# Performance work log

Measured on AMD Instinct MI355X. Metric: run time of the kernel, lower is better.

The kernel has to match this reference:

```python
import jax, jax.numpy as jnp
import numpy as np

B, T, E, D, H = 32, 2048, 512, 1024, 128

def setup_inputs() -> dict:
    key = jax.random.key(0)
    ks = jax.random.split(key, 8)
    encoder_outs = jax.random.normal(ks[0], (B, T, E), dtype=jnp.float32)
    decoder_state = jax.random.normal(ks[1], (B, D), dtype=jnp.float32)
    # valid lengths in [T//2, T]; mask=True on padded positions
    src_lens = jnp.clip(jax.random.randint(ks[2], (B,), 0, T), T // 2, T).astype(jnp.int32)
    mask = jnp.arange(T)[None, :] >= src_lens[:, None]  # [B,T] bool
    # parameters (nn.Linear style: y = x @ W^T + b; here stored pre-transposed)
    W_enc = jax.random.normal(ks[3], (E, H), dtype=jnp.float32) / np.sqrt(E)
    b_enc = jnp.zeros((H,), dtype=jnp.float32)
    W_dec = jax.random.normal(ks[4], (D, H), dtype=jnp.float32) / np.sqrt(D)  # bias=False
    w_w = jax.random.normal(ks[5], (H, 1), dtype=jnp.float32) / np.sqrt(H)
    w_b = jnp.zeros((1,), dtype=jnp.float32)
    return {"encoder_outs": encoder_outs, "src_lens": src_lens, "decoder_state": decoder_state,
            "mask": mask, "W_enc": W_enc, "b_enc": b_enc, "W_dec": W_dec, "w_w": w_w, "w_b": w_b}

def reference(encoder_outs, src_lens, decoder_state, mask, W_enc, b_enc, W_dec, w_w, w_b):
    # processed_memory = mlp_enc(encoder_outs): [B,T,H]
    processed = jnp.einsum('bte,eh->bth', encoder_outs, W_enc) + b_enc
    # mlp_dec(decoder_state).unsqueeze(1): [B,1,H]
    dec = (decoder_state @ W_dec)[:, None, :]
    # erg = w(tanh(processed + dec)).squeeze(-1): [B,T]
    erg = jnp.einsum('bth,h->bt', jnp.tanh(processed + dec), w_w[:, 0]) + w_b[0]
    erg = jnp.where(mask, -jnp.inf, erg)
    attention_weights = jax.nn.softmax(erg, axis=1)  # [B,T]
    attention_context = jnp.einsum('bte,bt->be', encoder_outs, attention_weights)  # [B,E]
    return attention_context, attention_weights
```

## Files before the change

### kernel.cpp

```cpp
#include <hip/hip_runtime.h>
#include <hip/hip_bf16.h>

#define B 32
#define T 2048
#define E 512
#define D 1024
#define H 128

typedef __attribute__((ext_vector_type(8))) short bf16x8;
typedef __attribute__((ext_vector_type(4))) float f32x4;

static __device__ __forceinline__ short f2b(float f) {
  __hip_bfloat16 h = __float2bfloat16(f);
  return __builtin_bit_cast(short, h);
}

__global__ __launch_bounds__(512) void prep_kernel(
    const float* __restrict__ ds, const float* __restrict__ Wd,
    const float* __restrict__ be, const float* __restrict__ We,
    float* __restrict__ dec_ws, char* __restrict__ WeT) {
  const int tid = threadIdx.x;
  if (blockIdx.x < 32) {
    const int b = blockIdx.x;
    const int h = tid & 127;
    const int kg = tid >> 7;
    __shared__ float sds[D];
    __shared__ float sred[4][H];
    for (int i = tid; i < D; i += 512) sds[i] = ds[b * D + i];
    __syncthreads();
    float acc = 0.0f;
    const int k0 = kg * 256;
#pragma unroll 8
    for (int k = k0; k < k0 + 256; ++k) acc = fmaf(sds[k], Wd[k * H + h], acc);
    sred[kg][h] = acc;
    __syncthreads();
    if (kg == 0)
      dec_ws[b * H + h] = be[h] + sred[0][h] + sred[1][h] + sred[2][h] + sred[3][h];
  } else {
    const int id = (blockIdx.x - 32) * 512 + tid;
    const int c = id >> 10;
    const int rem = id & 1023;
    const int h = rem & 127;
    const int s = rem >> 7;
    const int k0 = c * 64 + s * 8;
    bf16x8 v;
#pragma unroll
    for (int j = 0; j < 8; ++j) v[j] = f2b(We[(k0 + j) * H + h]);
    *(bf16x8*)(WeT + c * 16384 + h * 128 + ((s ^ (h & 7)) * 16)) = v;
  }
}

__global__ __launch_bounds__(1024, 1) void erg_mfma_kernel(
    const float* __restrict__ enc, const char* __restrict__ WeT,
    const float* __restrict__ dec_ws, const float* __restrict__ ww,
    const float* __restrict__ wb, float* __restrict__ erg_ws) {
  __shared__ __align__(16) char smem[131072];
  const int tid = threadIdx.x;
  const int lane = tid & 63;
  const int w = tid >> 6;
  const int m = lane & 15;
  const int g = lane >> 4;
  const int row0 = blockIdx.x * 256 + w * 16;
  const int b = row0 >> 11;

#pragma unroll
  for (int j = 0; j < 8; ++j)
    __builtin_amdgcn_global_load_lds(
        (const __attribute__((address_space(1))) void*)(WeT + j * 16384 + tid * 16),
        (__attribute__((address_space(3))) void*)(&smem[j * 16384 + tid * 16]),
        16, 0, 0);

  f32x4 acc[8];
#pragma unroll
  for (int n = 0; n < 8; ++n) {
    const float d = dec_ws[b * H + n * 16 + m];
    acc[n] = (f32x4){d, d, d, d};
  }

  const float* arow = enc + (size_t)(row0 + m) * E + g * 8;

  float4 a0 = *(const float4*)(arow);
  float4 a1 = *(const float4*)(arow + 4);
  float4 a2 = *(const float4*)(arow + 32);
  float4 a3 = *(const float4*)(arow + 36);

  asm volatile("s_waitcnt vmcnt(0)" ::: "memory");
  __syncthreads();

#pragma unroll
  for (int c = 0; c < 8; ++c) {
    float4 n0, n1, n2, n3;
    if (c < 7) {
      const float* ak = arow + (c + 1) * 64;
      n0 = *(const float4*)(ak);
      n1 = *(const float4*)(ak + 4);
      n2 = *(const float4*)(ak + 32);
      n3 = *(const float4*)(ak + 36);
    }
    bf16x8 af0, af1;
    af0[0] = f2b(a0.x); af0[1] = f2b(a0.y); af0[2] = f2b(a0.z); af0[3] = f2b(a0.w);
    af0[4] = f2b(a1.x); af0[5] = f2b(a1.y); af0[6] = f2b(a1.z); af0[7] = f2b(a1.w);
    af1[0] = f2b(a2.x); af1[1] = f2b(a2.y); af1[2] = f2b(a2.z); af1[3] = f2b(a2.w);
    af1[4] = f2b(a3.x); af1[5] = f2b(a3.y); af1[6] = f2b(a3.z); af1[7] = f2b(a3.w);

#pragma unroll
    for (int kk = 0; kk < 2; ++kk) {
      const int slot = (((kk * 4) + g) ^ (m & 7)) * 16;
      const bf16x8 af = kk ? af1 : af0;
#pragma unroll
      for (int n = 0; n < 8; ++n) {
        const bf16x8 bf =
            *(const bf16x8*)(&smem[c * 16384 + (n * 16 + m) * 128 + slot]);
        acc[n] = __builtin_amdgcn_mfma_f32_16x16x32_bf16(af, bf, acc[n], 0, 0, 0);
      }
    }
    a0 = n0; a1 = n1; a2 = n2; a3 = n3;
  }

  const float wbv = wb[0];
  float wwreg[8];
#pragma unroll
  for (int n = 0; n < 8; ++n) wwreg[n] = ww[n * 16 + m];
#pragma unroll
  for (int j = 0; j < 4; ++j) {
    float gsum = 0.0f;
#pragma unroll
    for (int n = 0; n < 8; ++n) {
      const float x = acc[n][j];
      const float th = 1.0f - 2.0f / (__expf(2.0f * x) + 1.0f);
      gsum = fmaf(wwreg[n], th, gsum);
    }
#pragma unroll
    for (int off = 1; off < 16; off <<= 1) gsum += __shfl_xor(gsum, off, 64);
    if (m == 0) erg_ws[row0 + g * 4 + j] = gsum + wbv;
  }
}

__global__ __launch_bounds__(1024, 1) void softmax_ctx_kernel(
    const float* __restrict__ enc, const float* __restrict__ erg_ws,
    const int* __restrict__ src_lens, float* __restrict__ w_out,
    float* __restrict__ ctx) {
  const int b = blockIdx.x;
  const int tid = threadIdx.x;
  const int lane = tid & 63, w = tid >> 6;
  const int n = src_lens[b];

  __shared__ float sw[T];
  __shared__ float red8[8][E];
  __shared__ float sred[16];
  __shared__ float sscal[2];

  const float x0 = erg_ws[b * T + tid];
  const float x1 = erg_ws[b * T + tid + 1024];
  const float v0 = (tid < n) ? x0 : -1e30f;
  const float v1 = (tid + 1024 < n) ? x1 : -1e30f;

  float mx = fmaxf(v0, v1);
#pragma unroll
  for (int off = 32; off > 0; off >>= 1) mx = fmaxf(mx, __shfl_xor(mx, off, 64));
  if (lane == 0) sred[w] = mx;
  __syncthreads();
  if (tid == 0) {
    float m2 = sred[0];
#pragma unroll
    for (int i = 1; i < 16; ++i) m2 = fmaxf(m2, sred[i]);
    sscal[0] = m2;
  }
  __syncthreads();
  mx = sscal[0];

  const float e0 = (v0 > -1e29f) ? __expf(v0 - mx) : 0.0f;
  const float e1 = (v1 > -1e29f) ? __expf(v1 - mx) : 0.0f;
  float s = e0 + e1;
#pragma unroll
  for (int off = 32; off > 0; off >>= 1) s += __shfl_xor(s, off, 64);
  if (lane == 0) sred[w] = s;
  __syncthreads();
  if (tid == 0) {
    float ss = 0.0f;
#pragma unroll
    for (int i = 0; i < 16; ++i) ss += sred[i];
    sscal[1] = 1.0f / ss;
  }
  __syncthreads();
  const float inv = sscal[1];

  const float w0 = e0 * inv, w1 = e1 * inv;
  w_out[b * T + tid] = w0;
  w_out[b * T + tid + 1024] = w1;
  sw[tid] = w0;
  sw[tid + 1024] = w1;
  __syncthreads();

  const int e4 = tid & 127;
  const int tg = tid >> 7;
  const float4* ep = (const float4*)(enc + ((size_t)b * T + tg * 256) * E) + e4;
  const float* swp = &sw[tg * 256];
  float4 acc = {0.0f, 0.0f, 0.0f, 0.0f};
#pragma unroll 8
  for (int i = 0; i < 256; ++i) {
    const float4 e = ep[(size_t)i * (E / 4)];
    const float wv = swp[i];
    acc.x = fmaf(e.x, wv, acc.x);
    acc.y = fmaf(e.y, wv, acc.y);
    acc.z = fmaf(e.z, wv, acc.z);
    acc.w = fmaf(e.w, wv, acc.w);
  }
  *(float4*)&red8[tg][e4 * 4] = acc;
  __syncthreads();
  if (tid < E) {
    float r = 0.0f;
#pragma unroll
    for (int p = 0; p < 8; ++p) r += red8[p][tid];
    ctx[b * E + tid] = r;
  }
}

extern "C" void kernel_launch(void* const* d_in, const int* in_sizes, int n_in,
                              void* d_out, int out_size, void* d_ws,
                              size_t ws_size, hipStream_t stream) {
  const float* enc = (const float*)d_in[0];
  const int* src_lens = (const int*)d_in[1];
  const float* ds = (const float*)d_in[2];
  const float* We = (const float*)d_in[4];
  const float* be = (const float*)d_in[5];
  const float* Wd = (const float*)d_in[6];
  const float* ww = (const float*)d_in[7];
  const float* wb = (const float*)d_in[8];

  float* ctx_out = (float*)d_out;
  float* w_out = (float*)d_out + B * E;

  float* ws = (float*)d_ws;
  float* dec_ws = ws;
  float* erg_ws = ws + B * H;
  char* WeT = (char*)(ws + B * H + B * T);

  prep_kernel<<<48, 512, 0, stream>>>(ds, Wd, be, We, dec_ws, WeT);
  erg_mfma_kernel<<<(B * T) / 256, 1024, 0, stream>>>(enc, WeT, dec_ws, ww, wb, erg_ws);
  softmax_ctx_kernel<<<B, 1024, 0, stream>>>(enc, erg_ws, src_lens, w_out, ctx_out);
}
```

Measured before the change: 273.2 us.

## Split softmax-context over time chunks with atomics and halve erg kernel LDS

The softmax/context kernel now runs a 32x32 grid of 128-thread blocks. Each block recomputes the row max and sum, then accumulates a 64-timestep slice of the context and adds it into the output with atomics. The output is zeroed in the prep kernel. This replaces 32 large blocks that each streamed a whole batch row, and is meant to spread the second pass over encoder_outs across all CUs. Separately, the erg MFMA kernel uses 512-thread blocks with 64KB of LDS and reloads the second half of the weights mid-loop, so several blocks can share a CU. The cost is redundant softmax reductions, float atomics with nondeterministic summation order, and an extra barrier and reload in the erg kernel.

Measured after the change: 249.9 us. 8.5% less time.

```diff
diff --git a/kernel.cpp b/kernel.cpp
--- a/kernel.cpp
+++ b/kernel.cpp
@@ -18,7 +18,8 @@
 __global__ __launch_bounds__(512) void prep_kernel(
     const float* __restrict__ ds, const float* __restrict__ Wd,
     const float* __restrict__ be, const float* __restrict__ We,
-    float* __restrict__ dec_ws, char* __restrict__ WeT) {
+    float* __restrict__ dec_ws, char* __restrict__ WeT,
+    float* __restrict__ ctx) {
   const int tid = threadIdx.x;
   if (blockIdx.x < 32) {
     const int b = blockIdx.x;
@@ -38,6 +39,8 @@
       dec_ws[b * H + h] = be[h] + sred[0][h] + sred[1][h] + sred[2][h] + sred[3][h];
   } else {
     const int id = (blockIdx.x - 32) * 512 + tid;
+    ctx[id * 2] = 0.0f;
+    ctx[id * 2 + 1] = 0.0f;
     const int c = id >> 10;
     const int rem = id & 1023;
     const int h = rem & 127;
@@ -50,24 +53,23 @@
   }
 }
 
-__global__ __launch_bounds__(1024, 1) void erg_mfma_kernel(
+__global__ __launch_bounds__(512, 4) void erg_mfma_kernel(
     const float* __restrict__ enc, const char* __restrict__ WeT,
     const float* __restrict__ dec_ws, const float* __restrict__ ww,
     const float* __restrict__ wb, float* __restrict__ erg_ws) {
-  __shared__ __align__(16) char smem[131072];
+  __shared__ __align__(16) char smem[65536];
   const int tid = threadIdx.x;
   const int lane = tid & 63;
-  const int w = tid >> 6;
   const int m = lane & 15;
   const int g = lane >> 4;
-  const int row0 = blockIdx.x * 256 + w * 16;
+  const int row0 = blockIdx.x * 128 + (tid >> 6) * 16;
   const int b = row0 >> 11;
 
 #pragma unroll
   for (int j = 0; j < 8; ++j)
     __builtin_amdgcn_global_load_lds(
-        (const __attribute__((address_space(1))) void*)(WeT + j * 16384 + tid * 16),
-        (__attribute__((address_space(3))) void*)(&smem[j * 16384 + tid * 16]),
+        (const __attribute__((address_space(1))) void*)(WeT + j * 8192 + tid * 16),
+        (__attribute__((address_space(3))) void*)(&smem[j * 8192 + tid * 16]),
         16, 0, 0);
 
   f32x4 acc[8];
@@ -103,6 +105,7 @@
     af1[0] = f2b(a2.x); af1[1] = f2b(a2.y); af1[2] = f2b(a2.z); af1[3] = f2b(a2.w);
     af1[4] = f2b(a3.x); af1[5] = f2b(a3.y); af1[6] = f2b(a3.z); af1[7] = f2b(a3.w);
 
+    const int lc = c & 3;
 #pragma unroll
     for (int kk = 0; kk < 2; ++kk) {
       const int slot = (((kk * 4) + g) ^ (m & 7)) * 16;
@@ -110,11 +113,23 @@
 #pragma unroll
       for (int n = 0; n < 8; ++n) {
         const bf16x8 bf =
-            *(const bf16x8*)(&smem[c * 16384 + (n * 16 + m) * 128 + slot]);
+            *(const bf16x8*)(&smem[lc * 16384 + (n * 16 + m) * 128 + slot]);
         acc[n] = __builtin_amdgcn_mfma_f32_16x16x32_bf16(af, bf, acc[n], 0, 0, 0);
       }
     }
     a0 = n0; a1 = n1; a2 = n2; a3 = n3;
+
+    if (c == 3) {
+      __syncthreads();
+#pragma unroll
+      for (int j = 0; j < 8; ++j)
+        __builtin_amdgcn_global_load_lds(
+            (const __attribute__((address_space(1))) void*)(WeT + 65536 + j * 8192 + tid * 16),
+            (__attribute__((address_space(3))) void*)(&smem[j * 8192 + tid * 16]),
+            16, 0, 0);
+      asm volatile("s_waitcnt vmcnt(0)" ::: "memory");
+      __syncthreads();
+    }
   }
 
   const float wbv = wb[0];
@@ -136,84 +151,78 @@
   }
 }
 
-__global__ __launch_bounds__(1024, 1) void softmax_ctx_kernel(
+__global__ __launch_bounds__(128) void softctx_kernel(
     const float* __restrict__ enc, const float* __restrict__ erg_ws,
     const int* __restrict__ src_lens, float* __restrict__ w_out,
     float* __restrict__ ctx) {
-  const int b = blockIdx.x;
+  const int b = blockIdx.y;
+  const int ch = blockIdx.x;
   const int tid = threadIdx.x;
   const int lane = tid & 63, w = tid >> 6;
   const int n = src_lens[b];
 
-  __shared__ float sw[T];
-  __shared__ float red8[8][E];
-  __shared__ float sred[16];
+  __shared__ float sred[2];
   __shared__ float sscal[2];
-
-  const float x0 = erg_ws[b * T + tid];
-  const float x1 = erg_ws[b * T + tid + 1024];
-  const float v0 = (tid < n) ? x0 : -1e30f;
-  const float v1 = (tid + 1024 < n) ? x1 : -1e30f;
-
-  float mx = fmaxf(v0, v1);
+  __shared__ float sw[64];
+
+  float v[16];
+  float mx = -1e30f;
+#pragma unroll
+  for (int i = 0; i < 16; ++i) {
+    const int t = tid + i * 128;
+    const float x = erg_ws[b * T + t];
+    v[i] = (t < n) ? x : -1e30f;
+    mx = fmaxf(mx, v[i]);
+  }
 #pragma unroll
   for (int off = 32; off > 0; off >>= 1) mx = fmaxf(mx, __shfl_xor(mx, off, 64));
   if (lane == 0) sred[w] = mx;
   __syncthreads();
-  if (tid == 0) {
-    float m2 = sred[0];
-#pragma unroll
-    for (int i = 1; i < 16; ++i) m2 = fmaxf(m2, sred[i]);
-    sscal[0] = m2;
-  }
-  __syncthreads();
-  mx = sscal[0];
-
-  const float e0 = (v0 > -1e29f) ? __expf(v0 - mx) : 0.0f;
-  const float e1 = (v1 > -1e29f) ? __expf(v1 - mx) : 0.0f;
-  float s = e0 + e1;
+  mx = fmaxf(sred[0], sred[1]);
+  __syncthreads();
+
+  float s = 0.0f;
+#pragma unroll
+  for (int i = 0; i < 16; ++i) {
+    v[i] = (v[i] > -1e29f) ? __expf(v[i] - mx) : 0.0f;
+    s += v[i];
+  }
 #pragma unroll
   for (int off = 32; off > 0; off >>= 1) s += __shfl_xor(s, off, 64);
   if (lane == 0) sred[w] = s;
   __syncthreads();
-  if (tid == 0) {
-    float ss = 0.0f;
-#pragma unroll
-    for (int i = 0; i < 16; ++i) ss += sred[i];
-    sscal[1] = 1.0f / ss;
-  }
-  __syncthreads();
-  const float inv = sscal[1];
-
-  const float w0 = e0 * inv, w1 = e1 * inv;
-  w_out[b * T + tid] = w0;
-  w_out[b * T + tid + 1024] = w1;
-  sw[tid] = w0;
-  sw[tid + 1024] = w1;
-  __syncthreads();
-
-  const int e4 = tid & 127;
-  const int tg = tid >> 7;
-  const float4* ep = (const float4*)(enc + ((size_t)b * T + tg * 256) * E) + e4;
-  const float* swp = &sw[tg * 256];
+  if (tid == 0) sscal[0] = 1.0f / (sred[0] + sred[1]);
+  __syncthreads();
+  const float inv = sscal[0];
+
+  if (ch == 0) {
+#pragma unroll
+    for (int i = 0; i < 16; ++i) w_out[b * T + tid + i * 128] = v[i] * inv;
+  }
+
+  if (tid < 64) {
+    const int t = ch * 64 + tid;
+    const float x = erg_ws[b * T + t];
+    sw[tid] = (t < n) ? __expf(x - mx) * inv : 0.0f;
+  }
+  __syncthreads();
+
+  const float4* ep = (const float4*)(enc + ((size_t)b * T + ch * 64) * E) + tid;
   float4 acc = {0.0f, 0.0f, 0.0f, 0.0f};
 #pragma unroll 8
-  for (int i = 0; i < 256; ++i) {
-    const float4 e = ep[(size_t)i * (E / 4)];
-    const float wv = swp[i];
+  for (int t = 0; t < 64; ++t) {
+    const float4 e = ep[(size_t)t * (E / 4)];
+    const float wv = sw[t];
     acc.x = fmaf(e.x, wv, acc.x);
     acc.y = fmaf(e.y, wv, acc.y);
     acc.z = fmaf(e.z, wv, acc.z);
     acc.w = fmaf(e.w, wv, acc.w);
   }
-  *(float4*)&red8[tg][e4 * 4] = acc;
-  __syncthreads();
-  if (tid < E) {
-    float r = 0.0f;
-#pragma unroll
-    for (int p = 0; p < 8; ++p) r += red8[p][tid];
-    ctx[b * E + tid] = r;
-  }
+  float* c = ctx + b * E + tid * 4;
+  atomicAdd(c + 0, acc.x);
+  atomicAdd(c + 1, acc.y);
+  atomicAdd(c + 2, acc.z);
+  atomicAdd(c + 3, acc.w);
 }
 
 extern "C" void kernel_launch(void* const* d_in, const int* in_sizes, int n_in,
@@ -236,7 +245,7 @@
   float* erg_ws = ws + B * H;
   char* WeT = (char*)(ws + B * H + B * T);
 
-  prep_kernel<<<48, 512, 0, stream>>>(ds, Wd, be, We, dec_ws, WeT);
-  erg_mfma_kernel<<<(B * T) / 256, 1024, 0, stream>>>(enc, WeT, dec_ws, ww, wb, erg_ws);
-  softmax_ctx_kernel<<<B, 1024, 0, stream>>>(enc, erg_ws, src_lens, w_out, ctx_out);
-}
+  prep_kernel<<<48, 512, 0, stream>>>(ds, Wd, be, We, dec_ws, WeT, ctx_out);
+  erg_mfma_kernel<<<(B * T) / 128, 512, 0, stream>>>(enc, WeT, dec_ws, ww, wb, erg_ws);
+  softctx_kernel<<<dim3(32, B), 128, 0, stream>>>(enc, erg_ws, src_lens, w_out, ctx_out);
+}
```
